# Kernel optimization log

Measured on AMD Instinct MI355X. Metric: run time of the kernel, lower is better.

Reference implementation:

```python
import jax, jax.numpy as jnp
import numpy as np

B = 32          # number of graphs
N_PER = 1000    # num_nodes per graph (CDSQN.num_nodes)
TOTAL = B * N_PER
E = 512000      # edges (avg degree 16)
F_IN = 128      # node_feat_dim
HID = 128       # hidden_dim (= GNN embedding_dim)
D = 64          # dsf_hidden_dim
NH = 3          # num_heads
EPS = 1e-6


def setup_inputs() -> dict:
    key = jax.random.key(0)
    ks = jax.random.split(key, 12)
    x = jax.random.normal(ks[0], (TOTAL, F_IN), jnp.float32)
    edge_index = jax.random.randint(ks[1], (2, E), 0, TOTAL, dtype=jnp.int64)
    batch_index = jnp.repeat(jnp.arange(B, dtype=jnp.int64), N_PER)
    actions = (jax.random.uniform(ks[2], (B, N_PER)) < 0.1).astype(jnp.float32)

    def lin(k, fan_in, fan_out):
        s = 1.0 / np.sqrt(fan_in)
        return jax.random.uniform(k, (fan_in, fan_out), jnp.float32, -s, s)

    Wc1 = lin(ks[3], F_IN, HID); bc1 = jnp.zeros((HID,), jnp.float32)
    Wc2 = lin(ks[4], HID, HID);  bc2 = jnp.zeros((HID,), jnp.float32)
    Wc3 = lin(ks[5], HID, HID);  bc3 = jnp.zeros((HID,), jnp.float32)
    Wg1 = lin(ks[6], HID, NH * N_PER * D); bg1 = jnp.full((NH * N_PER * D,), 0.1, jnp.float32)
    Wg2 = lin(ks[7], HID, NH * D * D);     bg2 = jnp.full((NH * D * D,), 0.1, jnp.float32)
    Wg3 = lin(ks[8], HID, NH * D);         bg3 = jnp.full((NH * D,), 0.1, jnp.float32)
    return dict(x=x, edge_index=edge_index, batch_index=batch_index, actions=actions,
                Wc1=Wc1, bc1=bc1, Wc2=Wc2, bc2=bc2, Wc3=Wc3, bc3=bc3,
                Wg1=Wg1, bg1=bg1, Wg2=Wg2, bg2=bg2, Wg3=Wg3, bg3=bg3)


def _gcn(h, W, b, src, dst, norm):
    # PyG GCNConv: h' = D^-1/2 (A+I) D^-1/2 (h W) + b ; src/dst include self loops
    h = h @ W
    msgs = h[src] * norm[:, None]            # [E+TOTAL, out]
    return jax.ops.segment_sum(msgs, dst, num_segments=TOTAL) + b


def reference(x, edge_index, batch_index, actions,
              Wc1, bc1, Wc2, bc2, Wc3, bc3,
              Wg1, bg1, Wg2, bg2, Wg3, bg3):
    loops = jnp.arange(TOTAL, dtype=edge_index.dtype)
    src = jnp.concatenate([edge_index[0], loops])
    dst = jnp.concatenate([edge_index[1], loops])
    deg = jax.ops.segment_sum(jnp.ones(src.shape[0], x.dtype), dst, num_segments=TOTAL)
    dinv = jnp.where(deg > 0, jax.lax.rsqrt(deg), 0.0)
    norm = dinv[src] * dinv[dst]

    h = jax.nn.relu(_gcn(x, Wc1, bc1, src, dst, norm))
    h = jax.nn.relu(_gcn(h, Wc2, bc2, src, dst, norm))
    h = _gcn(h, Wc3, bc3, src, dst, norm)

    # global_mean_pool
    cnt = jax.ops.segment_sum(jnp.ones(TOTAL, x.dtype), batch_index, num_segments=B)
    h_g = jax.ops.segment_sum(h, batch_index, num_segments=B) / cnt[:, None]  # [B, HID]

    # hypernetwork weights
    w1 = jax.nn.softplus((h_g @ Wg1 + bg1).reshape(B, NH, N_PER, D))
    w2 = jax.nn.softplus((h_g @ Wg2 + bg2).reshape(B, NH, D, D))
    w3 = jax.nn.softplus((h_g @ Wg3 + bg3).reshape(B, NH, D))

    # compute_q (2D actions branch)
    h1 = jnp.einsum('bn,bhnd->bhd', actions, w1)
    h1 = jnp.sqrt(jnp.clip(h1, 0.0) + EPS)           # SafeSqrt
    h2 = jnp.einsum('bhd,bhde->bhe', h1, w2)
    h2 = jnp.log1p(jnp.clip(h2, 0.0))                # SafeLog: log(1+clamp(x,0))
    out_heads = jnp.einsum('bhd,bhd->bh', h2, w3)    # [B, NH]
    return jnp.min(out_heads, axis=-1)               # [B]
```

## Files before the change

### kernel.cpp

```cpp
#include <hip/hip_runtime.h>
#include <hip/hip_bf16.h>
#include <math.h>

#define NB 32
#define N_PER 1000
#define TOTALN 32000
#define NE 512000
#define HID 128
#define Dh 64
#define NH 3
#define EPSV 1e-6f
#define PCH 25
#define W1CH 250

typedef __attribute__((ext_vector_type(8))) short bf16x8;
typedef __attribute__((ext_vector_type(4))) float f32x4;

__device__ __forceinline__ float softplusf(float x) {
    return fmaxf(x, 0.0f) + log1pf(expf(-fabsf(x)));
}
__device__ __forceinline__ unsigned short f2b(float f) {
    __hip_bfloat16 h = __float2bfloat16(f);
    return __builtin_bit_cast(unsigned short, h);
}
__device__ __forceinline__ float b2f(unsigned short u) {
    unsigned int x = ((unsigned int)u) << 16;
    return __builtin_bit_cast(float, x);
}

__global__ __launch_bounds__(256) void k_init_deg(float* deg) {
    int i = blockIdx.x * 256 + threadIdx.x;
    if (i < TOTALN) deg[i] = 1.0f;
}

__global__ __launch_bounds__(256) void k_deg(const int* __restrict__ ei, float* deg) {
    int e = blockIdx.x * 256 + threadIdx.x;
    if (e < NE) atomicAdd(&deg[ei[NE + e]], 1.0f);
}

__global__ __launch_bounds__(256) void k_prep(float* __restrict__ d, int* __restrict__ cnt) {
    int i = blockIdx.x * 256 + threadIdx.x;
    if (i < TOTALN) {
        float v = d[i];
        cnt[i] = (int)v - 1;
        d[i] = rsqrtf(v);
    }
}

__global__ __launch_bounds__(256) void k_scan_block(const int* __restrict__ cnt,
                                                    int* __restrict__ rowptr,
                                                    int* __restrict__ bsum) {
    __shared__ int sh[256];
    int t = threadIdx.x;
    int i = blockIdx.x * 256 + t;
    int v = cnt[i];
    sh[t] = v;
    __syncthreads();
    for (int off = 1; off < 256; off <<= 1) {
        int add = (t >= off) ? sh[t - off] : 0;
        __syncthreads();
        sh[t] += add;
        __syncthreads();
    }
    rowptr[i] = sh[t] - v;
    if (t == 255) bsum[blockIdx.x] = sh[255];
}

__global__ void k_scan_tot(int* __restrict__ bsum) {
    if (threadIdx.x == 0) {
        int run = 0;
        for (int i = 0; i < 125; ++i) { int t = bsum[i]; bsum[i] = run; run += t; }
    }
}

__global__ __launch_bounds__(256) void k_scan_add(int* __restrict__ rowptr,
                                                  const int* __restrict__ bsum,
                                                  int* __restrict__ cursor) {
    int i = blockIdx.x * 256 + threadIdx.x;
    int v = rowptr[i] + bsum[blockIdx.x];
    rowptr[i] = v;
    cursor[i] = v;
    if (i == 0) rowptr[TOTALN] = NE;
}

__global__ __launch_bounds__(256) void k_fill(const int* __restrict__ ei,
                                              const float* __restrict__ dinv,
                                              int* __restrict__ cursor,
                                              int* __restrict__ csr_src,
                                              float* __restrict__ csr_w) {
    int e = blockIdx.x * 256 + threadIdx.x;
    if (e < NE) {
        int s = ei[e], d = ei[NE + e];
        int pos = atomicAdd(&cursor[d], 1);
        csr_src[pos] = s;
        csr_w[pos] = dinv[s] * dinv[d];
    }
}

__global__ __launch_bounds__(256) void k_wcvt(const float* __restrict__ W,
                                              unsigned short* __restrict__ Wt) {
    int i = blockIdx.x * 256 + threadIdx.x;
    int k = i >> 7, c = i & 127;
    Wt[c * 128 + k] = f2b(W[i]);
}

template<int INF32>
__global__ __launch_bounds__(256) void k_mm(const void* __restrict__ Xv,
                                            const unsigned short* __restrict__ Wt,
                                            unsigned short* __restrict__ Y) {
    int tid = threadIdx.x;
    int wv = tid >> 6, l = tid & 63;
    int row0 = blockIdx.x * 64 + wv * 16;
    int r = l & 15, kc = l >> 4;
    bf16x8 a[4];
    if (INF32) {
        const float* X = (const float*)Xv;
#pragma unroll
        for (int ks = 0; ks < 4; ++ks) {
            const float* p = X + (long)(row0 + r) * 128 + ks * 32 + kc * 8;
            float4 f0 = *(const float4*)p;
            float4 f1 = *(const float4*)(p + 4);
            bf16x8 t;
            t[0] = (short)f2b(f0.x); t[1] = (short)f2b(f0.y);
            t[2] = (short)f2b(f0.z); t[3] = (short)f2b(f0.w);
            t[4] = (short)f2b(f1.x); t[5] = (short)f2b(f1.y);
            t[6] = (short)f2b(f1.z); t[7] = (short)f2b(f1.w);
            a[ks] = t;
        }
    } else {
        const unsigned short* X = (const unsigned short*)Xv;
#pragma unroll
        for (int ks = 0; ks < 4; ++ks)
            a[ks] = *(const bf16x8*)(X + (long)(row0 + r) * 128 + ks * 32 + kc * 8);
    }
    f32x4 acc[8];
#pragma unroll
    for (int nt = 0; nt < 8; ++nt) acc[nt] = (f32x4){0.f, 0.f, 0.f, 0.f};
#pragma unroll
    for (int ks = 0; ks < 4; ++ks) {
#pragma unroll
        for (int nt = 0; nt < 8; ++nt) {
            bf16x8 b = *(const bf16x8*)(Wt + (nt * 16 + r) * 128 + ks * 32 + kc * 8);
            acc[nt] = __builtin_amdgcn_mfma_f32_16x16x32_bf16(a[ks], b, acc[nt], 0, 0, 0);
        }
    }
#pragma unroll
    for (int nt = 0; nt < 8; ++nt)
#pragma unroll
        for (int j = 0; j < 4; ++j)
            Y[(long)(row0 + kc * 4 + j) * 128 + nt * 16 + r] = f2b(acc[nt][j]);
}

template<int MODE>
__global__ __launch_bounds__(256) void k_gather(const unsigned short* __restrict__ feat,
                                                unsigned short* __restrict__ out,
                                                const int* __restrict__ rowptr,
                                                const int* __restrict__ csr_src,
                                                const float* __restrict__ csr_w,
                                                const float* __restrict__ dinv,
                                                const float* __restrict__ bias) {
    int wid = threadIdx.x >> 6, lane = threadIdx.x & 63;
    int v = blockIdx.x * 4 + wid;
    const unsigned int* f2 = (const unsigned int*)feat;
    float dv = dinv[v];
    unsigned int sv = f2[v * 64 + lane];
    float acc0 = b2f((unsigned short)(sv & 0xffff)) * dv * dv;
    float acc1 = b2f((unsigned short)(sv >> 16)) * dv * dv;
    int e = rowptr[v], e1 = rowptr[v + 1];
    for (; e + 4 <= e1; e += 4) {
        int s0 = csr_src[e], s1 = csr_src[e + 1], s2 = csr_src[e + 2], s3 = csr_src[e + 3];
        float w0 = csr_w[e], w1 = csr_w[e + 1], w2 = csr_w[e + 2], w3 = csr_w[e + 3];
        unsigned int u0 = f2[s0 * 64 + lane];
        unsigned int u1 = f2[s1 * 64 + lane];
        unsigned int u2 = f2[s2 * 64 + lane];
        unsigned int u3 = f2[s3 * 64 + lane];
        acc0 += b2f((unsigned short)(u0 & 0xffff)) * w0 + b2f((unsigned short)(u1 & 0xffff)) * w1
              + b2f((unsigned short)(u2 & 0xffff)) * w2 + b2f((unsigned short)(u3 & 0xffff)) * w3;
        acc1 += b2f((unsigned short)(u0 >> 16)) * w0 + b2f((unsigned short)(u1 >> 16)) * w1
              + b2f((unsigned short)(u2 >> 16)) * w2 + b2f((unsigned short)(u3 >> 16)) * w3;
    }
    for (; e < e1; ++e) {
        int s = csr_src[e];
        float w = csr_w[e];
        unsigned int u = f2[s * 64 + lane];
        acc0 += b2f((unsigned short)(u & 0xffff)) * w;
        acc1 += b2f((unsigned short)(u >> 16)) * w;
    }
    if (MODE == 0) {
        int c = lane * 2;
        acc0 = fmaxf(acc0 + bias[c], 0.f);
        acc1 = fmaxf(acc1 + bias[c + 1], 0.f);
    }
    ((unsigned int*)out)[v * 64 + lane] =
        (unsigned int)f2b(acc0) | ((unsigned int)f2b(acc1) << 16);
}

__global__ __launch_bounds__(256) void k_pool1(const unsigned short* __restrict__ A,
                                               float* __restrict__ pp) {
    __shared__ float sh[256];
    int b = blockIdx.x / PCH, ch = blockIdx.x % PCH;
    int c = threadIdx.x & 127, half = threadIdx.x >> 7;
    float acc = 0.f;
    int n0 = ch * 40;
#pragma unroll 4
    for (int j = half; j < 40; j += 2)
        acc += b2f(A[(long)(b * N_PER + n0 + j) * 128 + c]);
    sh[threadIdx.x] = acc;
    __syncthreads();
    if (threadIdx.x < 128)
        pp[blockIdx.x * 128 + c] = sh[c] + sh[128 + c];
}

__global__ __launch_bounds__(256) void k_pool2(const float* __restrict__ pp,
                                               const float* __restrict__ bias,
                                               float* __restrict__ hg,
                                               float* __restrict__ hgT,
                                               unsigned short* __restrict__ hgB) {
    int i = blockIdx.x * 256 + threadIdx.x;
    if (i >= NB * 128) return;
    int b = i >> 7, c = i & 127;
    float s = 0.f;
#pragma unroll
    for (int ch = 0; ch < PCH; ++ch)
        s += pp[(b * PCH + ch) * 128 + c];
    float v = s * (1.0f / N_PER) + bias[c];
    hg[i] = v;
    hgT[c * NB + b] = v;
    hgB[i] = f2b(v);
}

__global__ __launch_bounds__(256) void k_w1(const unsigned short* __restrict__ hgB,
                                            const float* __restrict__ Wg1,
                                            const float* __restrict__ bg1,
                                            const float* __restrict__ actions,
                                            float* __restrict__ p1) {
    int h = blockIdx.x / W1CH, chunk = blockIdx.x % W1CH;
    int tid = threadIdx.x;
    int wv = tid >> 6, l = tid & 63;
    int r = l & 15, kc = l >> 4;
    int n = chunk * 4 + wv;
    const long KS = (long)NH * N_PER * Dh;
    long colbase = (long)h * (N_PER * Dh) + (long)n * Dh;
    bf16x8 a[2][4];
#pragma unroll
    for (int mt = 0; mt < 2; ++mt)
#pragma unroll
        for (int ks = 0; ks < 4; ++ks)
            a[mt][ks] = *(const bf16x8*)(hgB + (mt * 16 + r) * 128 + ks * 32 + kc * 8);
    f32x4 acc[2][4];
#pragma unroll
    for (int mt = 0; mt < 2; ++mt)
#pragma unroll
        for (int ct = 0; ct < 4; ++ct) acc[mt][ct] = (f32x4){0.f, 0.f, 0.f, 0.f};
#pragma unroll
    for (int ct = 0; ct < 4; ++ct) {
        const float* Wp = Wg1 + colbase + ct * 16 + r;
#pragma unroll
        for (int ks = 0; ks < 4; ++ks) {
            int kb = ks * 32 + kc * 8;
            float f0 = Wp[(long)(kb + 0) * KS];
            float f1 = Wp[(long)(kb + 1) * KS];
            float f2v = Wp[(long)(kb + 2) * KS];
            float f3 = Wp[(long)(kb + 3) * KS];
            float f4 = Wp[(long)(kb + 4) * KS];
            float f5 = Wp[(long)(kb + 5) * KS];
            float f6 = Wp[(long)(kb + 6) * KS];
            float f7 = Wp[(long)(kb + 7) * KS];
            bf16x8 bb;
            bb[0] = (short)f2b(f0); bb[1] = (short)f2b(f1);
            bb[2] = (short)f2b(f2v); bb[3] = (short)f2b(f3);
            bb[4] = (short)f2b(f4); bb[5] = (short)f2b(f5);
            bb[6] = (short)f2b(f6); bb[7] = (short)f2b(f7);
            acc[0][ct] = __builtin_amdgcn_mfma_f32_16x16x32_bf16(a[0][ks], bb, acc[0][ct], 0, 0, 0);
            acc[1][ct] = __builtin_amdgcn_mfma_f32_16x16x32_bf16(a[1][ks], bb, acc[1][ct], 0, 0, 0);
        }
    }
    float actv[2][4];
#pragma unroll
    for (int mt = 0; mt < 2; ++mt)
#pragma unroll
        for (int j = 0; j < 4; ++j)
            actv[mt][j] = actions[(mt * 16 + kc * 4 + j) * N_PER + n];
    float bgv[4];
#pragma unroll
    for (int ct = 0; ct < 4; ++ct)
        bgv[ct] = bg1[colbase + ct * 16 + r];
    float* po = p1 + ((long)h * N_PER + n) * 2048;
#pragma unroll
    for (int mt = 0; mt < 2; ++mt)
#pragma unroll
        for (int ct = 0; ct < 4; ++ct)
#pragma unroll
            for (int j = 0; j < 4; ++j) {
                int b = mt * 16 + kc * 4 + j;
                int d = ct * 16 + r;
                po[b * 64 + d] = softplusf(acc[mt][ct][j] + bgv[ct]) * actv[mt][j];
            }
}

__global__ __launch_bounds__(256) void k_red1(const float* __restrict__ p1,
                                              float* __restrict__ h1) {
    __shared__ float sh[4][64];
    int b = blockIdx.x / 3, h = blockIdx.x % 3;
    int part = threadIdx.x >> 6, d = threadIdx.x & 63;
    const float* base = p1 + (long)h * N_PER * 2048 + b * 64 + d;
    float s = 0.f;
#pragma unroll 4
    for (int n = part; n < N_PER; n += 4)
        s += base[(long)n * 2048];
    if (part) sh[part][d] = s;
    __syncthreads();
    if (part == 0)
        h1[(b * 3 + h) * 64 + d] = sqrtf(fmaxf(s + sh[1][d] + sh[2][d] + sh[3][d], 0.f) + EPSV);
}

__global__ __launch_bounds__(256) void k_w2(const float* __restrict__ hg,
                                            const float* __restrict__ Wg2,
                                            const float* __restrict__ bg2,
                                            const float* __restrict__ h1,
                                            float* __restrict__ p2) {
    __shared__ float hgs[32][128];
    __shared__ float wt[128][64];
    __shared__ float h1s[32];
    int hd = blockIdx.x;
    int tid = threadIdx.x;
    for (int i = 0; i < 16; ++i) {
        int idx = tid + i * 256;
        hgs[idx >> 7][idx & 127] = hg[idx];
    }
    long base = (long)hd * 64;
    for (int i = 0; i < 32; ++i) {
        int idx = tid + i * 256;
        wt[idx >> 6][idx & 63] = Wg2[(long)(idx >> 6) * (NH * Dh * Dh) + base + (idx & 63)];
    }
    int h = hd >> 6, d = hd & 63;
    if (tid < 32) h1s[tid] = h1[tid * (NH * Dh) + h * Dh + d];
    __syncthreads();
    int e = tid & 63, bq = tid >> 6;
    float bgv = bg2[base + e];
    float dot[8];
#pragma unroll
    for (int bi = 0; bi < 8; ++bi) dot[bi] = 0.f;
    for (int k = 0; k < 128; ++k) {
        float w = wt[k][e];
#pragma unroll
        for (int bi = 0; bi < 8; ++bi)
            dot[bi] += hgs[bq * 8 + bi][k] * w;
    }
    float* po = p2 + (long)hd * (32 * 64);
#pragma unroll
    for (int bi = 0; bi < 8; ++bi) {
        int b = bq * 8 + bi;
        po[b * 64 + e] = softplusf(dot[bi] + bgv) * h1s[b];
    }
}

__global__ __launch_bounds__(256) void k_red2(const float* __restrict__ p2,
                                              float* __restrict__ h2) {
    int o = blockIdx.x * 256 + threadIdx.x;
    if (o >= 32 * 192) return;
    int bh = o >> 6;
    int h = bh % 3, b = bh / 3;
    int e = o & 63;
    float s = 0.f;
    for (int d = 0; d < 64; ++d)
        s += p2[(h * 64 + d) * 2048 + b * 64 + e];
    h2[o] = log1pf(fmaxf(s, 0.f));
}

__global__ __launch_bounds__(192) void k_out(const float* __restrict__ hg,
                                             const float* __restrict__ Wg3,
                                             const float* __restrict__ bg3,
                                             const float* __restrict__ h2,
                                             float* __restrict__ out) {
    __shared__ float hgb[128];
    __shared__ float hres[NH];
    int b = blockIdx.x, tid = threadIdx.x;
    if (tid < 128) hgb[tid] = hg[b * 128 + tid];
    __syncthreads();
    int h = tid / 64, e = tid & 63;
    int c = h * 64 + e;
    float dot = 0.f;
    for (int k = 0; k < 128; ++k)
        dot += hgb[k] * Wg3[k * (NH * Dh) + c];
    float v = softplusf(dot + bg3[c]) * h2[b * 192 + c];
    for (int off = 32; off; off >>= 1)
        v += __shfl_down(v, off, 64);
    if (e == 0) hres[h] = v;
    __syncthreads();
    if (tid == 0) out[b] = fminf(fminf(hres[0], hres[1]), hres[2]);
}

extern "C" void kernel_launch(void* const* d_in, const int* in_sizes, int n_in,
                              void* d_out, int out_size, void* d_ws, size_t ws_size,
                              hipStream_t stream) {
    const float* x   = (const float*)d_in[0];
    const int*   ei  = (const int*)d_in[1];
    const float* act = (const float*)d_in[3];
    const float* Wc1 = (const float*)d_in[4];
    const float* bc1 = (const float*)d_in[5];
    const float* Wc2 = (const float*)d_in[6];
    const float* bc2 = (const float*)d_in[7];
    const float* Wc3 = (const float*)d_in[8];
    const float* bc3 = (const float*)d_in[9];
    const float* Wg1 = (const float*)d_in[10];
    const float* bg1 = (const float*)d_in[11];
    const float* Wg2 = (const float*)d_in[12];
    const float* bg2 = (const float*)d_in[13];
    const float* Wg3 = (const float*)d_in[14];
    const float* bg3 = (const float*)d_in[15];
    float* out = (float*)d_out;

    float* ws   = (float*)d_ws;
    float* dinv = ws;
    float* bufA = dinv + TOTALN;
    float* bufB = bufA + (long)TOTALN * 128;
    float* hg   = bufB + (long)TOTALN * 128;
    float* h1   = hg + 32 * 128;
    float* h2   = h1 + 32 * 192;
    float* csr_w = h2 + 32 * 192;
    float* pp   = csr_w + NE;
    float* hgT  = pp + NB * PCH * 128;
    unsigned short* hgB = (unsigned short*)(hgT + 128 * NB);
    int* cnt    = (int*)(hgB + 4096);
    int* rowptr = cnt + TOTALN;
    int* cursor = rowptr + TOTALN + 4;
    int* bsum   = cursor + TOTALN;
    int* csr_src= bsum + 128;
    unsigned short* Wt = (unsigned short*)(csr_src + NE);
    unsigned short* fA = (unsigned short*)bufA;
    unsigned short* fB = (unsigned short*)bufB;
    float* p1   = bufA;
    float* p2   = bufA + (long)3 * N_PER * 2048;

    k_init_deg<<<(TOTALN + 255) / 256, 256, 0, stream>>>(dinv);
    k_deg<<<NE / 256, 256, 0, stream>>>(ei, dinv);
    k_prep<<<(TOTALN + 255) / 256, 256, 0, stream>>>(dinv, cnt);
    k_scan_block<<<125, 256, 0, stream>>>(cnt, rowptr, bsum);
    k_scan_tot<<<1, 64, 0, stream>>>(bsum);
    k_scan_add<<<125, 256, 0, stream>>>(rowptr, bsum, cursor);
    k_fill<<<NE / 256, 256, 0, stream>>>(ei, dinv, cursor, csr_src, csr_w);

    k_wcvt<<<64, 256, 0, stream>>>(Wc1, Wt);
    k_mm<1><<<500, 256, 0, stream>>>(x, Wt, fB);
    k_gather<0><<<TOTALN / 4, 256, 0, stream>>>(fB, fA, rowptr, csr_src, csr_w, dinv, bc1);
    k_wcvt<<<64, 256, 0, stream>>>(Wc2, Wt);
    k_mm<0><<<500, 256, 0, stream>>>(fA, Wt, fB);
    k_gather<0><<<TOTALN / 4, 256, 0, stream>>>(fB, fA, rowptr, csr_src, csr_w, dinv, bc2);
    k_wcvt<<<64, 256, 0, stream>>>(Wc3, Wt);
    k_mm<0><<<500, 256, 0, stream>>>(fA, Wt, fB);
    k_gather<1><<<TOTALN / 4, 256, 0, stream>>>(fB, fA, rowptr, csr_src, csr_w, dinv, nullptr);
    k_pool1<<<NB * PCH, 256, 0, stream>>>(fA, pp);
    k_pool2<<<(NB * 128 + 255) / 256, 256, 0, stream>>>(pp, bc3, hg, hgT, hgB);

    k_w1<<<NH * W1CH, 256, 0, stream>>>(hgB, Wg1, bg1, act, p1);
    k_red1<<<96, 256, 0, stream>>>(p1, h1);
    k_w2<<<NH * Dh, 256, 0, stream>>>(hg, Wg2, bg2, h1, p2);
    k_red2<<<24, 256, 0, stream>>>(p2, h2);
    k_out<<<NB, 192, 0, stream>>>(hg, Wg3, bg3, h2, out);
}
```

Measured before the change: 281.6 us.

## Stage Wg1 tiles through LDS for coalesced loads and split red1 reduction

k_w1 now has each block cooperatively load one 128x64 Wg1 tile per node into shared memory, with consecutive threads reading consecutive columns, then converts it to bf16 and feeds the MFMA operands from LDS. Before, each lane read scattered 16-wide strided column segments. The idea is to coalesce the dominant 24.6M-float weight stream, at the cost of block-wide barriers and serialising four nodes per block. The k_red1 reduction is also split into two kernels: 768 blocks produce partial sums over segments and a second kernel combines them. This raises parallelism over the 96-block version at the price of one extra launch and a scratch buffer that reuses pp.

```diff
diff --git a/kernel.cpp b/kernel.cpp
--- a/kernel.cpp
+++ b/kernel.cpp
@@ -234,84 +234,76 @@
                                             const float* __restrict__ bg1,
                                             const float* __restrict__ actions,
                                             float* __restrict__ p1) {
+    __shared__ unsigned short wt[64][136];
     int h = blockIdx.x / W1CH, chunk = blockIdx.x % W1CH;
     int tid = threadIdx.x;
     int wv = tid >> 6, l = tid & 63;
     int r = l & 15, kc = l >> 4;
-    int n = chunk * 4 + wv;
     const long KS = (long)NH * N_PER * Dh;
-    long colbase = (long)h * (N_PER * Dh) + (long)n * Dh;
     bf16x8 a[2][4];
 #pragma unroll
     for (int mt = 0; mt < 2; ++mt)
 #pragma unroll
         for (int ks = 0; ks < 4; ++ks)
             a[mt][ks] = *(const bf16x8*)(hgB + (mt * 16 + r) * 128 + ks * 32 + kc * 8);
-    f32x4 acc[2][4];
-#pragma unroll
-    for (int mt = 0; mt < 2; ++mt)
-#pragma unroll
-        for (int ct = 0; ct < 4; ++ct) acc[mt][ct] = (f32x4){0.f, 0.f, 0.f, 0.f};
-#pragma unroll
-    for (int ct = 0; ct < 4; ++ct) {
-        const float* Wp = Wg1 + colbase + ct * 16 + r;
+    int sd = tid & 63, sk = tid >> 6;
+    for (int nn = 0; nn < 4; ++nn) {
+        int n = chunk * 4 + nn;
+        long colbase = (long)h * (N_PER * Dh) + (long)n * Dh;
+        __syncthreads();
+        const float* Wb = Wg1 + colbase + sd;
+#pragma unroll 8
+        for (int it = 0; it < 32; ++it) {
+            int k = it * 4 + sk;
+            wt[sd][k] = f2b(Wb[(long)k * KS]);
+        }
+        __syncthreads();
+        f32x4 acc0 = (f32x4){0.f, 0.f, 0.f, 0.f};
+        f32x4 acc1 = (f32x4){0.f, 0.f, 0.f, 0.f};
 #pragma unroll
         for (int ks = 0; ks < 4; ++ks) {
-            int kb = ks * 32 + kc * 8;
-            float f0 = Wp[(long)(kb + 0) * KS];
-            float f1 = Wp[(long)(kb + 1) * KS];
-            float f2v = Wp[(long)(kb + 2) * KS];
-            float f3 = Wp[(long)(kb + 3) * KS];
-            float f4 = Wp[(long)(kb + 4) * KS];
-            float f5 = Wp[(long)(kb + 5) * KS];
-            float f6 = Wp[(long)(kb + 6) * KS];
-            float f7 = Wp[(long)(kb + 7) * KS];
-            bf16x8 bb;
-            bb[0] = (short)f2b(f0); bb[1] = (short)f2b(f1);
-            bb[2] = (short)f2b(f2v); bb[3] = (short)f2b(f3);
-            bb[4] = (short)f2b(f4); bb[5] = (short)f2b(f5);
-            bb[6] = (short)f2b(f6); bb[7] = (short)f2b(f7);
-            acc[0][ct] = __builtin_amdgcn_mfma_f32_16x16x32_bf16(a[0][ks], bb, acc[0][ct], 0, 0, 0);
-            acc[1][ct] = __builtin_amdgcn_mfma_f32_16x16x32_bf16(a[1][ks], bb, acc[1][ct], 0, 0, 0);
+            bf16x8 bb = *(const bf16x8*)&wt[wv * 16 + r][ks * 32 + kc * 8];
+            acc0 = __builtin_amdgcn_mfma_f32_16x16x32_bf16(a[0][ks], bb, acc0, 0, 0, 0);
+            acc1 = __builtin_amdgcn_mfma_f32_16x16x32_bf16(a[1][ks], bb, acc1, 0, 0, 0);
         }
-    }
-    float actv[2][4];
-#pragma unroll
-    for (int mt = 0; mt < 2; ++mt)
-#pragma unroll
-        for (int j = 0; j < 4; ++j)
-            actv[mt][j] = actions[(mt * 16 + kc * 4 + j) * N_PER + n];
-    float bgv[4];
-#pragma unroll
-    for (int ct = 0; ct < 4; ++ct)
-        bgv[ct] = bg1[colbase + ct * 16 + r];
-    float* po = p1 + ((long)h * N_PER + n) * 2048;
-#pragma unroll
-    for (int mt = 0; mt < 2; ++mt)
-#pragma unroll
-        for (int ct = 0; ct < 4; ++ct)
-#pragma unroll
-            for (int j = 0; j < 4; ++j) {
-                int b = mt * 16 + kc * 4 + j;
-                int d = ct * 16 + r;
-                po[b * 64 + d] = softplusf(acc[mt][ct][j] + bgv[ct]) * actv[mt][j];
-            }
-}
-
-__global__ __launch_bounds__(256) void k_red1(const float* __restrict__ p1,
-                                              float* __restrict__ h1) {
+        float bgv = bg1[colbase + wv * 16 + r];
+        float* po = p1 + ((long)h * N_PER + n) * 2048;
+#pragma unroll
+        for (int j = 0; j < 4; ++j) {
+            int b0 = kc * 4 + j;
+            int b1 = 16 + kc * 4 + j;
+            po[b0 * 64 + wv * 16 + r] = softplusf(acc0[j] + bgv) * actions[b0 * N_PER + n];
+            po[b1 * 64 + wv * 16 + r] = softplusf(acc1[j] + bgv) * actions[b1 * N_PER + n];
+        }
+    }
+}
+
+__global__ __launch_bounds__(256) void k_red1a(const float* __restrict__ p1,
+                                               float* __restrict__ rp) {
     __shared__ float sh[4][64];
-    int b = blockIdx.x / 3, h = blockIdx.x % 3;
+    int bh = blockIdx.x >> 3, seg = blockIdx.x & 7;
+    int b = bh / 3, h = bh % 3;
     int part = threadIdx.x >> 6, d = threadIdx.x & 63;
     const float* base = p1 + (long)h * N_PER * 2048 + b * 64 + d;
     float s = 0.f;
-#pragma unroll 4
-    for (int n = part; n < N_PER; n += 4)
+    for (int n = seg * 125 + part; n < seg * 125 + 125; n += 4)
         s += base[(long)n * 2048];
     if (part) sh[part][d] = s;
     __syncthreads();
     if (part == 0)
-        h1[(b * 3 + h) * 64 + d] = sqrtf(fmaxf(s + sh[1][d] + sh[2][d] + sh[3][d], 0.f) + EPSV);
+        rp[((long)bh * 8 + seg) * 64 + d] = s + sh[1][d] + sh[2][d] + sh[3][d];
+}
+
+__global__ __launch_bounds__(256) void k_red1b(const float* __restrict__ rp,
+                                               float* __restrict__ h1) {
+    int o = blockIdx.x * 256 + threadIdx.x;
+    if (o >= 96 * 64) return;
+    int bh = o >> 6, d = o & 63;
+    float s = 0.f;
+#pragma unroll
+    for (int seg = 0; seg < 8; ++seg)
+        s += rp[((long)bh * 8 + seg) * 64 + d];
+    h1[bh * 64 + d] = sqrtf(fmaxf(s, 0.f) + EPSV);
 }
 
 __global__ __launch_bounds__(256) void k_w2(const float* __restrict__ hg,
@@ -432,6 +424,7 @@
     unsigned short* fB = (unsigned short*)bufB;
     float* p1   = bufA;
     float* p2   = bufA + (long)3 * N_PER * 2048;
+    float* rp   = pp;
 
     k_init_deg<<<(TOTALN + 255) / 256, 256, 0, stream>>>(dinv);
     k_deg<<<NE / 256, 256, 0, stream>>>(ei, dinv);
@@ -454,7 +447,8 @@
     k_pool2<<<(NB * 128 + 255) / 256, 256, 0, stream>>>(pp, bc3, hg, hgT, hgB);
 
     k_w1<<<NH * W1CH, 256, 0, stream>>>(hgB, Wg1, bg1, act, p1);
-    k_red1<<<96, 256, 0, stream>>>(p1, h1);
+    k_red1a<<<96 * 8, 256, 0, stream>>>(p1, rp);
+    k_red1b<<<24, 256, 0, stream>>>(rp, h1);
     k_w2<<<NH * Dh, 256, 0, stream>>>(hg, Wg2, bg2, h1, p2);
     k_red2<<<24, 256, 0, stream>>>(p2, h2);
     k_out<<<NB, 192, 0, stream>>>(hg, Wg3, bg3, h2, out);
```

Result: faster. 270.9 us (-3.8%).
